# Kernel tuning notes

Measured on AMD Instinct MI355X. Metric: run time of the kernel, lower is better.

The kernel has to match this reference:

```python
import jax, jax.numpy as jnp
import numpy as np

VOCAB, EMBED, HIDDEN, NCLS = 50257, 1024, 4096, 3
B, S = 4096, 128


def ternary_quant(w):
    # Per-tensor ternary quantization: scale = mean |w|, weights in {-s, 0, +s}.
    s = jnp.mean(jnp.abs(w))
    return jnp.round(jnp.clip(w / s, -1.0, 1.0)) * s


def layer_norm(x, g, b, eps=1e-5):
    mu = jnp.mean(x, axis=-1, keepdims=True)
    var = jnp.mean(jnp.square(x - mu), axis=-1, keepdims=True)
    return (x - mu) * jax.lax.rsqrt(var + eps) * g + b


def setup_inputs() -> dict:
    key = jax.random.key(0)
    ks = jax.random.split(key, 12)
    input_ids = jax.random.randint(ks[0], (B, S), 0, VOCAB, dtype=jnp.int32)
    emb = jax.random.normal(ks[1], (VOCAB, EMBED), dtype=jnp.float32) * 0.02
    emb = emb.at[0].set(0.0)  # padding_idx=0
    w1 = jax.random.normal(ks[2], (HIDDEN, EMBED), dtype=jnp.float32) * 0.02
    b1 = jnp.zeros((HIDDEN,), jnp.float32)
    w2 = jax.random.normal(ks[3], (HIDDEN // 2, HIDDEN), dtype=jnp.float32) * 0.02
    b2 = jnp.zeros((HIDDEN // 2,), jnp.float32)
    w3 = jax.random.normal(ks[4], (NCLS, HIDDEN // 2), dtype=jnp.float32) * 0.02
    b3 = jnp.zeros((NCLS,), jnp.float32)
    g1 = jnp.ones((HIDDEN,), jnp.float32)
    beta1 = jnp.zeros((HIDDEN,), jnp.float32)
    g2 = jnp.ones((HIDDEN // 2,), jnp.float32)
    beta2 = jnp.zeros((HIDDEN // 2,), jnp.float32)
    return dict(input_ids=input_ids, emb=emb, w1=w1, b1=b1, w2=w2, b2=b2,
                w3=w3, b3=b3, g1=g1, beta1=beta1, g2=g2, beta2=beta2)


def reference(input_ids, emb, w1, b1, w2, b2, w3, b3, g1, beta1, g2, beta2):
    x = emb[input_ids]                                   # (B, S, E)
    mask = (input_ids != 0).astype(x.dtype)[..., None]   # (B, S, 1)
    x = jnp.sum(x * mask, axis=1) / jnp.clip(jnp.sum(mask, axis=1), 1.0)  # (B, E)
    h = jax.nn.gelu(layer_norm(x @ ternary_quant(w1).T + b1, g1, beta1), approximate=False)
    h = jax.nn.gelu(layer_norm(h @ ternary_quant(w2).T + b2, g2, beta2), approximate=False)
    logits = h @ ternary_quant(w3).T + b3                # (B, 3)
    return logits
```

## Files before the change

kernel.cpp:

```cpp
#include <hip/hip_runtime.h>
#include <cstdint>
#include <cstddef>


#define GAS __attribute__((address_space(1)))
#define LAS __attribute__((address_space(3)))

typedef __bf16 bf16x8 __attribute__((ext_vector_type(8)));
typedef float  f32x4  __attribute__((ext_vector_type(4)));
typedef unsigned short u16x8 __attribute__((ext_vector_type(8)));

__device__ __forceinline__ unsigned short f2bf(float f) {
    unsigned int u = __float_as_uint(f);
    u += 0x7FFFu + ((u >> 16) & 1u);
    return (unsigned short)(u >> 16);
}
__device__ __forceinline__ float bf2f(unsigned short h) {
    return __uint_as_float(((unsigned int)h) << 16);
}

static constexpr int BB = 4096;
static constexpr int SS = 128;
static constexpr int EE = 1024;
static constexpr int HH = 4096;
static constexpr int H2D = 2048;
static constexpr int VOCAB = 50257;

static constexpr size_t OFF_S    = 0;
static constexpr size_t OFF_X    = 4096;
static constexpr size_t SZ_X     = (size_t)BB * EE * 2;
static constexpr size_t OFF_EMBH = OFF_X + SZ_X;
static constexpr size_t SZ_EMBH  = (size_t)VOCAB * EE * 2;
static constexpr size_t OFF_Q1   = OFF_EMBH;
static constexpr size_t OFF_Q2   = OFF_Q1 + (size_t)HH * EE * 2;
static constexpr size_t OFF_C    = OFF_Q2 + (size_t)H2D * HH * 2;
static constexpr size_t OFF_H1   = OFF_EMBH + SZ_EMBH;
static constexpr size_t OFF_H2   = OFF_Q1;


__global__ void zero_sums(double* s) {
    if (threadIdx.x < 3) s[threadIdx.x] = 0.0;
}

__global__ __launch_bounds__(256) void prep_kernel(const float* __restrict__ e,
                                                   unsigned short* __restrict__ o,
                                                   const float* __restrict__ w1,
                                                   const float* __restrict__ w2,
                                                   const float* __restrict__ w3,
                                                   double* __restrict__ sums) {
    const int bid = blockIdx.x;
    const int tid = threadIdx.x;
    if (bid < 4096) {
        const int n8 = (VOCAB * EE) / 8;
        for (int i = bid * 256 + tid; i < n8; i += 4096 * 256) {
            const float4 v0 = ((const float4*)e)[2 * i];
            const float4 v1 = ((const float4*)e)[2 * i + 1];
            union { unsigned short u[8]; uint4 q; } r;
            r.u[0] = f2bf(v0.x); r.u[1] = f2bf(v0.y); r.u[2] = f2bf(v0.z); r.u[3] = f2bf(v0.w);
            r.u[4] = f2bf(v1.x); r.u[5] = f2bf(v1.y); r.u[6] = f2bf(v1.z); r.u[7] = f2bf(v1.w);
            ((uint4*)o)[i] = r.q;
        }
        return;
    }
    const float* w; int n; double* out; int b0; int nb;
    if (bid < 5120)      { w = w1; n = HH * EE;  out = sums + 0; b0 = bid - 4096; nb = 1024; }
    else if (bid < 7168) { w = w2; n = H2D * HH; out = sums + 1; b0 = bid - 5120; nb = 2048; }
    else                 { w = w3; n = 3 * H2D;  out = sums + 2; b0 = bid - 7168; nb = 24;   }
    const int lane = tid & 63, wid = tid >> 6;
    double acc = 0.0;
    for (int i = b0 * 256 + tid; i < n; i += nb * 256)
        acc += (double)fabsf(w[i]);
    for (int off = 32; off; off >>= 1) acc += __shfl_down(acc, off);
    __shared__ double r[4];
    if (lane == 0) r[wid] = acc;
    __syncthreads();
    if (tid == 0) atomicAdd(out, r[0] + r[1] + r[2] + r[3]);
}

__global__ __launch_bounds__(256) void quant_all(const float* __restrict__ w1,
                                                 const float* __restrict__ w2,
                                                 const double* __restrict__ sums,
                                                 unsigned short* __restrict__ q1,
                                                 unsigned short* __restrict__ q2) {
    const int bid = blockIdx.x;
    const float* w; int n; unsigned short* q; int b0; int nb; double ssum; double dn;
    if (bid < 4096) { w = w1; n = HH * EE;  q = q1; b0 = bid;        nb = 4096; ssum = sums[0]; dn = (double)(HH) * EE; }
    else            { w = w2; n = H2D * HH; q = q2; b0 = bid - 4096; nb = 8192; ssum = sums[1]; dn = (double)(H2D) * HH; }
    const float inv_s = (float)(dn / ssum);
    for (int i = b0 * 256 + threadIdx.x; i < n; i += nb * 256) {
        float t = w[i] * inv_s;
        t = fminf(1.f, fmaxf(-1.f, t));
        q[i] = f2bf(rintf(t));
    }
}

__global__ __launch_bounds__(256) void pool_kernel(const int* __restrict__ ids,
                                                   const unsigned short* __restrict__ embh,
                                                   unsigned short* __restrict__ X) {
    const int tid = threadIdx.x;
    const int row = tid >> 7;
    const int t   = tid & 127;
    __shared__ int sid[256];
    __shared__ int sorted_ids[2][128];
    __shared__ int cnt[2][64];
    __shared__ int pos[2][64];
    __shared__ int nz[2];
    sid[tid] = ids[(size_t)blockIdx.x * 256 + tid];
    if (tid < 128) ((int*)cnt)[tid] = 0;
    if (tid < 2) nz[tid] = 0;
    __syncthreads();
    const int myid = sid[tid];
    const int ph = myid >> 10;
    atomicAdd(&cnt[row][ph], 1);
    if (myid != 0) atomicAdd(&nz[row], 1);
    __syncthreads();
    if (tid < 2) {
        int s = 0;
        #pragma unroll
        for (int p = 0; p < 64; ++p) { pos[tid][p] = s; s += cnt[tid][p]; }
    }
    __syncthreads();
    const int where = atomicAdd(&pos[row][ph], 1);
    sorted_ids[row][where] = myid;
    __syncthreads();

    const int col = t * 8;
    float a[8] = {};
    #pragma unroll 8
    for (int s = 0; s < 128; ++s) {
        const int id = sorted_ids[row][s];
        const u16x8 v = *(const u16x8*)(embh + (size_t)id * EE + col);
        #pragma unroll
        for (int j = 0; j < 8; ++j) a[j] += bf2f(v[j]);
    }
    const int c = nz[row];
    const float inv = 1.f / (float)(c ? c : 1);
    u16x8 ov;
    #pragma unroll
    for (int j = 0; j < 8; ++j) ov[j] = f2bf(a[j] * inv);
    const int b = blockIdx.x * 2 + row;
    *(u16x8*)(X + (size_t)b * EE + col) = ov;
}

__global__ __launch_bounds__(256) void gemm_bt(const unsigned short* __restrict__ A,
                                               const unsigned short* __restrict__ B,
                                               float* __restrict__ C, int M, int N, int K) {
    __shared__ unsigned short sA[128 * 32];
    __shared__ unsigned short sB[128 * 32];
    const int tid  = threadIdx.x;
    const int wid  = tid >> 6;
    const int lane = tid & 63;
    const int wm = wid >> 1, wn = wid & 1;
    const int quad = lane >> 4;
    const int l16  = lane & 15;
    const int mBase = blockIdx.y * 128;
    const int nBase = blockIdx.x * 128;

    f32x4 acc[4][4] = {};

    const int srow = tid >> 2;
    const int scol = (tid & 3) * 8;
    const size_t aOff0 = (size_t)(mBase + srow) * K + scol;
    const size_t aOff1 = aOff0 + (size_t)64 * K;
    const size_t bOff0 = (size_t)(nBase + srow) * K + scol;
    const size_t bOff1 = bOff0 + (size_t)64 * K;
    unsigned short* ldsA0 = &sA[wid * 512];
    unsigned short* ldsA1 = &sA[2048 + wid * 512];
    unsigned short* ldsB0 = &sB[wid * 512];
    unsigned short* ldsB1 = &sB[2048 + wid * 512];

    for (int k0 = 0; k0 < K; k0 += 32) {
        __syncthreads();
        __builtin_amdgcn_global_load_lds((const GAS void*)(A + aOff0 + k0), (LAS void*)ldsA0, 16, 0, 0);
        __builtin_amdgcn_global_load_lds((const GAS void*)(A + aOff1 + k0), (LAS void*)ldsA1, 16, 0, 0);
        __builtin_amdgcn_global_load_lds((const GAS void*)(B + bOff0 + k0), (LAS void*)ldsB0, 16, 0, 0);
        __builtin_amdgcn_global_load_lds((const GAS void*)(B + bOff1 + k0), (LAS void*)ldsB1, 16, 0, 0);
        __syncthreads();

        bf16x8 af[4], bfr[4];
        #pragma unroll
        for (int i = 0; i < 4; ++i) {
            const int rowA = wm * 64 + i * 16 + l16;
            af[i]  = *(const bf16x8*)(&sA[rowA * 32 + quad * 8]);
            const int rowB = wn * 64 + i * 16 + l16;
            bfr[i] = *(const bf16x8*)(&sB[rowB * 32 + quad * 8]);
        }
        #pragma unroll
        for (int i = 0; i < 4; ++i)
            #pragma unroll
            for (int j = 0; j < 4; ++j)
                acc[i][j] = __builtin_amdgcn_mfma_f32_16x16x32_bf16(af[i], bfr[j], acc[i][j], 0, 0, 0);
    }

    #pragma unroll
    for (int i = 0; i < 4; ++i) {
        const int row0 = mBase + wm * 64 + i * 16 + quad * 4;
        #pragma unroll
        for (int j = 0; j < 4; ++j) {
            const int col = nBase + wn * 64 + j * 16 + l16;
            #pragma unroll
            for (int r = 0; r < 4; ++r)
                C[(size_t)(row0 + r) * N + col] = acc[i][j][r];
        }
    }
}

__global__ __launch_bounds__(256) void ln_gelu_kernel(const float* __restrict__ Cm,
                                                      const double* __restrict__ ssum, double nw,
                                                      const float* __restrict__ bias,
                                                      const float* __restrict__ gamma,
                                                      const float* __restrict__ beta,
                                                      unsigned short* __restrict__ H, int N) {
    __shared__ float buf[4096];
    __shared__ float redS[4], redQ[4];
    const int row = blockIdx.x, tid = threadIdx.x;
    const int lane = tid & 63, wid = tid >> 6;
    const float s = (float)(ssum[0] / nw);
    float ps = 0.f, pq = 0.f;
    for (int c = tid; c < N; c += 256) {
        const float y = Cm[(size_t)row * N + c] * s + bias[c];
        buf[c] = y;
        ps += y; pq += y * y;
    }
    for (int o = 32; o; o >>= 1) { ps += __shfl_down(ps, o); pq += __shfl_down(pq, o); }
    if (lane == 0) { redS[wid] = ps; redQ[wid] = pq; }
    __syncthreads();
    const float sum = redS[0] + redS[1] + redS[2] + redS[3];
    const float sq  = redQ[0] + redQ[1] + redQ[2] + redQ[3];
    const float mu  = sum / (float)N;
    float var = sq / (float)N - mu * mu;
    var = fmaxf(var, 0.f);
    const float inv = rsqrtf(var + 1e-5f);
    for (int c = tid; c < N; c += 256) {
        const float y = (buf[c] - mu) * inv * gamma[c] + beta[c];
        const float g = 0.5f * y * (1.f + erff(y * 0.70710678118654752f));
        H[(size_t)row * N + c] = f2bf(g);
    }
}

__global__ __launch_bounds__(256) void final_kernel(const unsigned short* __restrict__ H2,
                                                    const float* __restrict__ w3,
                                                    const double* __restrict__ ssum,
                                                    const float* __restrict__ b3,
                                                    float* __restrict__ out) {
    const int row = blockIdx.x, tid = threadIdx.x;
    const int lane = tid & 63, wid = tid >> 6;
    const float inv_s3 = (float)((double)(3 * H2D) / ssum[0]);
    float a0 = 0.f, a1 = 0.f, a2 = 0.f;
    for (int k = tid; k < H2D; k += 256) {
        const float h = bf2f(H2[(size_t)row * H2D + k]);
        const float q0 = rintf(fminf(1.f, fmaxf(-1.f, w3[k] * inv_s3)));
        const float q1 = rintf(fminf(1.f, fmaxf(-1.f, w3[H2D + k] * inv_s3)));
        const float q2 = rintf(fminf(1.f, fmaxf(-1.f, w3[2 * H2D + k] * inv_s3)));
        a0 += h * q0; a1 += h * q1; a2 += h * q2;
    }
    for (int o = 32; o; o >>= 1) {
        a0 += __shfl_down(a0, o); a1 += __shfl_down(a1, o); a2 += __shfl_down(a2, o);
    }
    __shared__ float r[3][4];
    if (lane == 0) { r[0][wid] = a0; r[1][wid] = a1; r[2][wid] = a2; }
    __syncthreads();
    if (tid < 3) {
        const float s3 = (float)(ssum[0] / (double)(3 * H2D));
        out[(size_t)row * 3 + tid] =
            (r[tid][0] + r[tid][1] + r[tid][2] + r[tid][3]) * s3 + b3[tid];
    }
}


extern "C" void kernel_launch(void* const* d_in, const int* in_sizes, int n_in,
                              void* d_out, int out_size, void* d_ws, size_t ws_size,
                              hipStream_t stream) {
    const int*   ids = (const int*)d_in[0];
    const float* emb = (const float*)d_in[1];
    const float* w1  = (const float*)d_in[2];
    const float* b1  = (const float*)d_in[3];
    const float* w2  = (const float*)d_in[4];
    const float* b2  = (const float*)d_in[5];
    const float* w3  = (const float*)d_in[6];
    const float* b3  = (const float*)d_in[7];
    const float* g1  = (const float*)d_in[8];
    const float* be1 = (const float*)d_in[9];
    const float* g2  = (const float*)d_in[10];
    const float* be2 = (const float*)d_in[11];
    float* out = (float*)d_out;
    char* ws = (char*)d_ws;

    double*         sums = (double*)(ws + OFF_S);
    unsigned short* X    = (unsigned short*)(ws + OFF_X);
    unsigned short* embh = (unsigned short*)(ws + OFF_EMBH);
    unsigned short* q1   = (unsigned short*)(ws + OFF_Q1);
    unsigned short* q2   = (unsigned short*)(ws + OFF_Q2);
    float*          Cbuf = (float*)(ws + OFF_C);
    unsigned short* H1   = (unsigned short*)(ws + OFF_H1);
    unsigned short* H2   = (unsigned short*)(ws + OFF_H2);

    zero_sums<<<1, 64, 0, stream>>>(sums);
    prep_kernel<<<7192, 256, 0, stream>>>(emb, embh, w1, w2, w3, sums);
    pool_kernel<<<BB / 2, 256, 0, stream>>>(ids, embh, X);

    quant_all<<<12288, 256, 0, stream>>>(w1, w2, sums, q1, q2);

    gemm_bt<<<dim3(HH / 128, BB / 128), 256, 0, stream>>>(X, q1, Cbuf, BB, HH, EE);
    ln_gelu_kernel<<<BB, 256, 0, stream>>>(Cbuf, sums + 0, (double)HH * (double)EE,
                                           b1, g1, be1, H1, HH);
    gemm_bt<<<dim3(H2D / 128, BB / 128), 256, 0, stream>>>(H1, q2, Cbuf, BB, H2D, HH);
    ln_gelu_kernel<<<BB, 256, 0, stream>>>(Cbuf, sums + 1, (double)H2D * (double)HH,
                                           b2, g2, be2, H2, H2D);
    final_kernel<<<BB, 256, 0, stream>>>(H2, w3, sums + 2, b3, out);
}
```

Baseline: 723.0 us.

## Split-K second GEMM, bf16 first-GEMM output, and two-stage abs-sum reductions

```diff
diff --git a/kernel.cpp b/kernel.cpp
--- a/kernel.cpp
+++ b/kernel.cpp
@@ -26,55 +26,77 @@
 static constexpr int H2D = 2048;
 static constexpr int VOCAB = 50257;
 
+static constexpr size_t MiB      = 1024 * 1024;
 static constexpr size_t OFF_S    = 0;
-static constexpr size_t OFF_X    = 4096;
-static constexpr size_t SZ_X     = (size_t)BB * EE * 2;
-static constexpr size_t OFF_EMBH = OFF_X + SZ_X;
+static constexpr size_t OFF_X    = 65536;
+static constexpr size_t OFF_EMBH = OFF_X + (size_t)BB * EE * 2;
 static constexpr size_t SZ_EMBH  = (size_t)VOCAB * EE * 2;
 static constexpr size_t OFF_Q1   = OFF_EMBH;
-static constexpr size_t OFF_Q2   = OFF_Q1 + (size_t)HH * EE * 2;
-static constexpr size_t OFF_C    = OFF_Q2 + (size_t)H2D * HH * 2;
+static constexpr size_t OFF_Q2   = OFF_EMBH + 8 * MiB;
+static constexpr size_t OFF_C1   = OFF_EMBH + 24 * MiB;
+static constexpr size_t OFF_C2   = OFF_EMBH + 24 * MiB;
+static constexpr size_t OFF_H2   = OFF_EMBH;
 static constexpr size_t OFF_H1   = OFF_EMBH + SZ_EMBH;
-static constexpr size_t OFF_H2   = OFF_Q1;
-
-
-__global__ void zero_sums(double* s) {
-    if (threadIdx.x < 3) s[threadIdx.x] = 0.0;
-}
-
-__global__ __launch_bounds__(256) void prep_kernel(const float* __restrict__ e,
-                                                   unsigned short* __restrict__ o,
-                                                   const float* __restrict__ w1,
-                                                   const float* __restrict__ w2,
+
+
+__global__ __launch_bounds__(256) void prep2_kernel(const float* __restrict__ e,
+                                                    unsigned short* __restrict__ o,
+                                                    const float* __restrict__ w1,
+                                                    const float* __restrict__ w2,
+                                                    double* __restrict__ part1,
+                                                    double* __restrict__ part2) {
+    const int bid = blockIdx.x;
+    const int tid = threadIdx.x;
+    const int n8 = (VOCAB * EE) / 8;
+    for (int i = bid * 256 + tid; i < n8; i += 2048 * 256) {
+        const float4 v0 = ((const float4*)e)[2 * i];
+        const float4 v1 = ((const float4*)e)[2 * i + 1];
+        union { unsigned short u[8]; uint4 q; } r;
+        r.u[0] = f2bf(v0.x); r.u[1] = f2bf(v0.y); r.u[2] = f2bf(v0.z); r.u[3] = f2bf(v0.w);
+        r.u[4] = f2bf(v1.x); r.u[5] = f2bf(v1.y); r.u[6] = f2bf(v1.z); r.u[7] = f2bf(v1.w);
+        ((uint4*)o)[i] = r.q;
+    }
+    const int lane = tid & 63, wid = tid >> 6;
+    double a1 = 0.0, a2 = 0.0;
+    const int n41 = HH * EE / 4;
+    for (int i = bid * 256 + tid; i < n41; i += 2048 * 256) {
+        const float4 v = ((const float4*)w1)[i];
+        a1 += (double)fabsf(v.x) + (double)fabsf(v.y) + (double)fabsf(v.z) + (double)fabsf(v.w);
+    }
+    const int n42 = H2D * HH / 4;
+    for (int i = bid * 256 + tid; i < n42; i += 2048 * 256) {
+        const float4 v = ((const float4*)w2)[i];
+        a2 += (double)fabsf(v.x) + (double)fabsf(v.y) + (double)fabsf(v.z) + (double)fabsf(v.w);
+    }
+    for (int off = 32; off; off >>= 1) { a1 += __shfl_down(a1, off); a2 += __shfl_down(a2, off); }
+    __shared__ double r1[4], r2[4];
+    if (lane == 0) { r1[wid] = a1; r2[wid] = a2; }
+    __syncthreads();
+    if (tid == 0) {
+        part1[bid] = r1[0] + r1[1] + r1[2] + r1[3];
+        part2[bid] = r2[0] + r2[1] + r2[2] + r2[3];
+    }
+}
+
+__global__ __launch_bounds__(256) void reduce_sums(const double* __restrict__ part1,
+                                                   const double* __restrict__ part2,
                                                    const float* __restrict__ w3,
                                                    double* __restrict__ sums) {
-    const int bid = blockIdx.x;
-    const int tid = threadIdx.x;
-    if (bid < 4096) {
-        const int n8 = (VOCAB * EE) / 8;
-        for (int i = bid * 256 + tid; i < n8; i += 4096 * 256) {
-            const float4 v0 = ((const float4*)e)[2 * i];
-            const float4 v1 = ((const float4*)e)[2 * i + 1];
-            union { unsigned short u[8]; uint4 q; } r;
-            r.u[0] = f2bf(v0.x); r.u[1] = f2bf(v0.y); r.u[2] = f2bf(v0.z); r.u[3] = f2bf(v0.w);
-            r.u[4] = f2bf(v1.x); r.u[5] = f2bf(v1.y); r.u[6] = f2bf(v1.z); r.u[7] = f2bf(v1.w);
-            ((uint4*)o)[i] = r.q;
-        }
-        return;
-    }
-    const float* w; int n; double* out; int b0; int nb;
-    if (bid < 5120)      { w = w1; n = HH * EE;  out = sums + 0; b0 = bid - 4096; nb = 1024; }
-    else if (bid < 7168) { w = w2; n = H2D * HH; out = sums + 1; b0 = bid - 5120; nb = 2048; }
-    else                 { w = w3; n = 3 * H2D;  out = sums + 2; b0 = bid - 7168; nb = 24;   }
+    const int bid = blockIdx.x, tid = threadIdx.x;
     const int lane = tid & 63, wid = tid >> 6;
     double acc = 0.0;
-    for (int i = b0 * 256 + tid; i < n; i += nb * 256)
-        acc += (double)fabsf(w[i]);
-    for (int off = 32; off; off >>= 1) acc += __shfl_down(acc, off);
+    if (bid == 0) {
+        for (int i = tid; i < 2048; i += 256) acc += part1[i];
+    } else if (bid == 1) {
+        for (int i = tid; i < 2048; i += 256) acc += part2[i];
+    } else {
+        for (int i = tid; i < 3 * H2D; i += 256) acc += (double)fabsf(w3[i]);
+    }
+    for (int o = 32; o; o >>= 1) acc += __shfl_down(acc, o);
     __shared__ double r[4];
     if (lane == 0) r[wid] = acc;
     __syncthreads();
-    if (tid == 0) atomicAdd(out, r[0] + r[1] + r[2] + r[3]);
+    if (tid == 0) sums[bid] = r[0] + r[1] + r[2] + r[3];
 }
 
 __global__ __launch_bounds__(256) void quant_all(const float* __restrict__ w1,
@@ -83,14 +105,19 @@
                                                  unsigned short* __restrict__ q1,
                                                  unsigned short* __restrict__ q2) {
     const int bid = blockIdx.x;
-    const float* w; int n; unsigned short* q; int b0; int nb; double ssum; double dn;
-    if (bid < 4096) { w = w1; n = HH * EE;  q = q1; b0 = bid;        nb = 4096; ssum = sums[0]; dn = (double)(HH) * EE; }
-    else            { w = w2; n = H2D * HH; q = q2; b0 = bid - 4096; nb = 8192; ssum = sums[1]; dn = (double)(H2D) * HH; }
+    const float* w; int n8; unsigned short* q; int b0; int nb; double ssum; double dn;
+    if (bid < 2048) { w = w1; n8 = HH * EE / 8;  q = q1; b0 = bid;        nb = 2048; ssum = sums[0]; dn = (double)HH * EE;  }
+    else            { w = w2; n8 = H2D * HH / 8; q = q2; b0 = bid - 2048; nb = 4096; ssum = sums[1]; dn = (double)H2D * HH; }
     const float inv_s = (float)(dn / ssum);
-    for (int i = b0 * 256 + threadIdx.x; i < n; i += nb * 256) {
-        float t = w[i] * inv_s;
-        t = fminf(1.f, fmaxf(-1.f, t));
-        q[i] = f2bf(rintf(t));
+    for (int i = b0 * 256 + threadIdx.x; i < n8; i += nb * 256) {
+        const float4 v0 = ((const float4*)w)[2 * i];
+        const float4 v1 = ((const float4*)w)[2 * i + 1];
+        union { unsigned short u[8]; uint4 p; } r;
+        const float a[8] = {v0.x, v0.y, v0.z, v0.w, v1.x, v1.y, v1.z, v1.w};
+        #pragma unroll
+        for (int j = 0; j < 8; ++j)
+            r.u[j] = f2bf(rintf(fminf(1.f, fmaxf(-1.f, a[j] * inv_s))));
+        ((uint4*)q)[i] = r.p;
     }
 }
 
@@ -142,56 +169,76 @@
     *(u16x8*)(X + (size_t)b * EE + col) = ov;
 }
 
-__global__ __launch_bounds__(256) void gemm_bt(const unsigned short* __restrict__ A,
-                                               const unsigned short* __restrict__ B,
-                                               float* __restrict__ C, int M, int N, int K) {
-    __shared__ unsigned short sA[128 * 32];
-    __shared__ unsigned short sB[128 * 32];
-    const int tid  = threadIdx.x;
-    const int wid  = tid >> 6;
-    const int lane = tid & 63;
-    const int wm = wid >> 1, wn = wid & 1;
-    const int quad = lane >> 4;
-    const int l16  = lane & 15;
-    const int mBase = blockIdx.y * 128;
-    const int nBase = blockIdx.x * 128;
-
-    f32x4 acc[4][4] = {};
-
-    const int srow = tid >> 2;
-    const int scol = (tid & 3) * 8;
-    const size_t aOff0 = (size_t)(mBase + srow) * K + scol;
-    const size_t aOff1 = aOff0 + (size_t)64 * K;
-    const size_t bOff0 = (size_t)(nBase + srow) * K + scol;
-    const size_t bOff1 = bOff0 + (size_t)64 * K;
-    unsigned short* ldsA0 = &sA[wid * 512];
-    unsigned short* ldsA1 = &sA[2048 + wid * 512];
-    unsigned short* ldsB0 = &sB[wid * 512];
-    unsigned short* ldsB1 = &sB[2048 + wid * 512];
-
-    for (int k0 = 0; k0 < K; k0 += 32) {
-        __syncthreads();
-        __builtin_amdgcn_global_load_lds((const GAS void*)(A + aOff0 + k0), (LAS void*)ldsA0, 16, 0, 0);
-        __builtin_amdgcn_global_load_lds((const GAS void*)(A + aOff1 + k0), (LAS void*)ldsA1, 16, 0, 0);
-        __builtin_amdgcn_global_load_lds((const GAS void*)(B + bOff0 + k0), (LAS void*)ldsB0, 16, 0, 0);
-        __builtin_amdgcn_global_load_lds((const GAS void*)(B + bOff1 + k0), (LAS void*)ldsB1, 16, 0, 0);
-        __syncthreads();
-
-        bf16x8 af[4], bfr[4];
-        #pragma unroll
-        for (int i = 0; i < 4; ++i) {
-            const int rowA = wm * 64 + i * 16 + l16;
-            af[i]  = *(const bf16x8*)(&sA[rowA * 32 + quad * 8]);
-            const int rowB = wn * 64 + i * 16 + l16;
-            bfr[i] = *(const bf16x8*)(&sB[rowB * 32 + quad * 8]);
+#define GEMM_BODY(K_START, K_END)                                                            \
+    __shared__ unsigned short sA[128 * 32];                                                  \
+    __shared__ unsigned short sB[128 * 32];                                                  \
+    const int tid  = threadIdx.x;                                                            \
+    const int wid  = tid >> 6;                                                               \
+    const int lane = tid & 63;                                                               \
+    const int wm = wid >> 1, wn = wid & 1;                                                   \
+    const int quad = lane >> 4;                                                              \
+    const int l16  = lane & 15;                                                              \
+    const int mBase = blockIdx.y * 128;                                                      \
+    const int nBase = blockIdx.x * 128;                                                      \
+    f32x4 acc[4][4] = {};                                                                    \
+    const int srow = tid >> 2;                                                               \
+    const int scol = (tid & 3) * 8;                                                          \
+    const size_t aOff0 = (size_t)(mBase + srow) * K + scol;                                  \
+    const size_t aOff1 = aOff0 + (size_t)64 * K;                                             \
+    const size_t bOff0 = (size_t)(nBase + srow) * K + scol;                                  \
+    const size_t bOff1 = bOff0 + (size_t)64 * K;                                             \
+    unsigned short* ldsA0 = &sA[wid * 512];                                                  \
+    unsigned short* ldsA1 = &sA[2048 + wid * 512];                                           \
+    unsigned short* ldsB0 = &sB[wid * 512];                                                  \
+    unsigned short* ldsB1 = &sB[2048 + wid * 512];                                           \
+    for (int k0 = (K_START); k0 < (K_END); k0 += 32) {                                       \
+        __syncthreads();                                                                     \
+        __builtin_amdgcn_global_load_lds((const GAS void*)(A + aOff0 + k0), (LAS void*)ldsA0, 16, 0, 0); \
+        __builtin_amdgcn_global_load_lds((const GAS void*)(A + aOff1 + k0), (LAS void*)ldsA1, 16, 0, 0); \
+        __builtin_amdgcn_global_load_lds((const GAS void*)(B + bOff0 + k0), (LAS void*)ldsB0, 16, 0, 0); \
+        __builtin_amdgcn_global_load_lds((const GAS void*)(B + bOff1 + k0), (LAS void*)ldsB1, 16, 0, 0); \
+        __syncthreads();                                                                     \
+        bf16x8 af[4], bfr[4];                                                                \
+        _Pragma("unroll")                                                                    \
+        for (int i = 0; i < 4; ++i) {                                                        \
+            const int rowA = wm * 64 + i * 16 + l16;                                         \
+            af[i]  = *(const bf16x8*)(&sA[rowA * 32 + quad * 8]);                            \
+            const int rowB = wn * 64 + i * 16 + l16;                                         \
+            bfr[i] = *(const bf16x8*)(&sB[rowB * 32 + quad * 8]);                            \
+        }                                                                                    \
+        _Pragma("unroll")                                                                    \
+        for (int i = 0; i < 4; ++i)                                                          \
+            _Pragma("unroll")                                                                \
+            for (int j = 0; j < 4; ++j)                                                      \
+                acc[i][j] = __builtin_amdgcn_mfma_f32_16x16x32_bf16(af[i], bfr[j], acc[i][j], 0, 0, 0); \
+    }
+
+__global__ __launch_bounds__(256) void gemm_bt_c16(const unsigned short* __restrict__ A,
+                                                   const unsigned short* __restrict__ B,
+                                                   unsigned short* __restrict__ C,
+                                                   int M, int N, int K) {
+    GEMM_BODY(0, K)
+    #pragma unroll
+    for (int i = 0; i < 4; ++i) {
+        const int row0 = mBase + wm * 64 + i * 16 + quad * 4;
+        #pragma unroll
+        for (int j = 0; j < 4; ++j) {
+            const int col = nBase + wn * 64 + j * 16 + l16;
+            #pragma unroll
+            for (int r = 0; r < 4; ++r)
+                C[(size_t)(row0 + r) * N + col] = f2bf(acc[i][j][r]);
         }
-        #pragma unroll
-        for (int i = 0; i < 4; ++i)
-            #pragma unroll
-            for (int j = 0; j < 4; ++j)
-                acc[i][j] = __builtin_amdgcn_mfma_f32_16x16x32_bf16(af[i], bfr[j], acc[i][j], 0, 0, 0);
-    }
-
+    }
+}
+
+__global__ __launch_bounds__(256) void gemm_bt_sk2(const unsigned short* __restrict__ A,
+                                                   const unsigned short* __restrict__ B,
+                                                   float* __restrict__ Cp,
+                                                   int M, int N, int K) {
+    const int kHalf = K >> 1;
+    const int kStart = blockIdx.z * kHalf;
+    float* C = Cp + (size_t)blockIdx.z * M * N;
+    GEMM_BODY(kStart, kStart + kHalf)
     #pragma unroll
     for (int i = 0; i < 4; ++i) {
         const int row0 = mBase + wm * 64 + i * 16 + quad * 4;
@@ -205,12 +252,12 @@
     }
 }
 
-__global__ __launch_bounds__(256) void ln_gelu_kernel(const float* __restrict__ Cm,
-                                                      const double* __restrict__ ssum, double nw,
-                                                      const float* __restrict__ bias,
-                                                      const float* __restrict__ gamma,
-                                                      const float* __restrict__ beta,
-                                                      unsigned short* __restrict__ H, int N) {
+__global__ __launch_bounds__(256) void ln_gelu_c16(const unsigned short* __restrict__ Cm,
+                                                   const double* __restrict__ ssum, double nw,
+                                                   const float* __restrict__ bias,
+                                                   const float* __restrict__ gamma,
+                                                   const float* __restrict__ beta,
+                                                   unsigned short* __restrict__ H, int N) {
     __shared__ float buf[4096];
     __shared__ float redS[4], redQ[4];
     const int row = blockIdx.x, tid = threadIdx.x;
@@ -218,7 +265,42 @@
     const float s = (float)(ssum[0] / nw);
     float ps = 0.f, pq = 0.f;
     for (int c = tid; c < N; c += 256) {
-        const float y = Cm[(size_t)row * N + c] * s + bias[c];
+        const float y = bf2f(Cm[(size_t)row * N + c]) * s + bias[c];
+        buf[c] = y;
+        ps += y; pq += y * y;
+    }
+    for (int o = 32; o; o >>= 1) { ps += __shfl_down(ps, o); pq += __shfl_down(pq, o); }
+    if (lane == 0) { redS[wid] = ps; redQ[wid] = pq; }
+    __syncthreads();
+    const float sum = redS[0] + redS[1] + redS[2] + redS[3];
+    const float sq  = redQ[0] + redQ[1] + redQ[2] + redQ[3];
+    const float mu  = sum / (float)N;
+    float var = sq / (float)N - mu * mu;
+    var = fmaxf(var, 0.f);
+    const float inv = rsqrtf(var + 1e-5f);
+    for (int c = tid; c < N; c += 256) {
+        const float y = (buf[c] - mu) * inv * gamma[c] + beta[c];
+        const float g = 0.5f * y * (1.f + erff(y * 0.70710678118654752f));
+        H[(size_t)row * N + c] = f2bf(g);
+    }
+}
+
+__global__ __launch_bounds__(256) void ln_gelu_2buf(const float* __restrict__ Ca,
+                                                    const float* __restrict__ Cb,
+                                                    const double* __restrict__ ssum, double nw,
+                                                    const float* __restrict__ bias,
+                                                    const float* __restrict__ gamma,
+                                                    const float* __restrict__ beta,
+                                                    unsigned short* __restrict__ H, int N) {
+    __shared__ float buf[2048];
+    __shared__ float redS[4], redQ[4];
+    const int row = blockIdx.x, tid = threadIdx.x;
+    const int lane = tid & 63, wid = tid >> 6;
+    const float s = (float)(ssum[0] / nw);
+    float ps = 0.f, pq = 0.f;
+    for (int c = tid; c < N; c += 256) {
+        const size_t idx = (size_t)row * N + c;
+        const float y = (Ca[idx] + Cb[idx]) * s + bias[c];
         buf[c] = y;
         ps += y; pq += y * y;
     }
@@ -286,26 +368,29 @@
     float* out = (float*)d_out;
     char* ws = (char*)d_ws;
 
-    double*         sums = (double*)(ws + OFF_S);
-    unsigned short* X    = (unsigned short*)(ws + OFF_X);
-    unsigned short* embh = (unsigned short*)(ws + OFF_EMBH);
-    unsigned short* q1   = (unsigned short*)(ws + OFF_Q1);
-    unsigned short* q2   = (unsigned short*)(ws + OFF_Q2);
-    float*          Cbuf = (float*)(ws + OFF_C);
-    unsigned short* H1   = (unsigned short*)(ws + OFF_H1);
-    unsigned short* H2   = (unsigned short*)(ws + OFF_H2);
-
-    zero_sums<<<1, 64, 0, stream>>>(sums);
-    prep_kernel<<<7192, 256, 0, stream>>>(emb, embh, w1, w2, w3, sums);
+    double*         sums  = (double*)(ws + OFF_S);
+    double*         part1 = sums + 8;
+    double*         part2 = part1 + 2048;
+    unsigned short* X     = (unsigned short*)(ws + OFF_X);
+    unsigned short* embh  = (unsigned short*)(ws + OFF_EMBH);
+    unsigned short* q1    = (unsigned short*)(ws + OFF_Q1);
+    unsigned short* q2    = (unsigned short*)(ws + OFF_Q2);
+    unsigned short* C1    = (unsigned short*)(ws + OFF_C1);
+    float*          Cp    = (float*)(ws + OFF_C2);
+    unsigned short* H1    = (unsigned short*)(ws + OFF_H1);
+    unsigned short* H2    = (unsigned short*)(ws + OFF_H2);
+
+    prep2_kernel<<<2048, 256, 0, stream>>>(emb, embh, w1, w2, part1, part2);
+    reduce_sums<<<3, 256, 0, stream>>>(part1, part2, w3, sums);
     pool_kernel<<<BB / 2, 256, 0, stream>>>(ids, embh, X);
 
-    quant_all<<<12288, 256, 0, stream>>>(w1, w2, sums, q1, q2);
-
-    gemm_bt<<<dim3(HH / 128, BB / 128), 256, 0, stream>>>(X, q1, Cbuf, BB, HH, EE);
-    ln_gelu_kernel<<<BB, 256, 0, stream>>>(Cbuf, sums + 0, (double)HH * (double)EE,
-                                           b1, g1, be1, H1, HH);
-    gemm_bt<<<dim3(H2D / 128, BB / 128), 256, 0, stream>>>(H1, q2, Cbuf, BB, H2D, HH);
-    ln_gelu_kernel<<<BB, 256, 0, stream>>>(Cbuf, sums + 1, (double)H2D * (double)HH,
-                                           b2, g2, be2, H2, H2D);
+    quant_all<<<6144, 256, 0, stream>>>(w1, w2, sums, q1, q2);
+
+    gemm_bt_c16<<<dim3(HH / 128, BB / 128), 256, 0, stream>>>(X, q1, C1, BB, HH, EE);
+    ln_gelu_c16<<<BB, 256, 0, stream>>>(C1, sums + 0, (double)HH * (double)EE,
+                                        b1, g1, be1, H1, HH);
+    gemm_bt_sk2<<<dim3(H2D / 128, BB / 128, 2), 256, 0, stream>>>(H1, q2, Cp, BB, H2D, HH);
+    ln_gelu_2buf<<<BB, 256, 0, stream>>>(Cp, Cp + (size_t)BB * H2D, sums + 1,
+                                         (double)H2D * (double)HH, b2, g2, be2, H2, H2D);
     final_kernel<<<BB, 256, 0, stream>>>(H2, w3, sums + 2, b3, out);
 }
```

Measured after the change: 709.2 us. About the same (-1.9%).
